# Performance work log

Measured on AMD Instinct MI355X. Metric: run time of the kernel, lower is better.

## Reference

```python
import jax, jax.numpy as jnp
import numpy as np
import math

D_SINGLE, D_PAIR, H, PQ, PV = 384, 128, 12, 4, 8
DH = D_SINGLE // H
OUT_DIM = H * DH + H * PV * 4 + H * D_PAIR


def setup_inputs() -> dict:
    key = jax.random.key(0)
    ks = jax.random.split(key, 24)
    B, L = 1, 512
    inp = {
        'single': jax.random.normal(ks[0], (B, L, D_SINGLE), jnp.float32),
        'pair': jax.random.normal(ks[1], (B, L, L, D_PAIR), jnp.float32),
        'rot_mats': jax.random.normal(ks[2], (B, L, 3, 3), jnp.float32),
        'trans': jax.random.normal(ks[3], (B, L, 3), jnp.float32),
        'mask': jnp.ones((B, L), jnp.float32),
        'ln_w': jnp.ones((D_SINGLE,), jnp.float32),
        'ln_b': jnp.zeros((D_SINGLE,), jnp.float32),
        'Wq': jax.random.normal(ks[4], (D_SINGLE, H * DH), jnp.float32) * 0.02,
        'bq': jnp.zeros((H * DH,), jnp.float32),
        'Wk': jax.random.normal(ks[5], (D_SINGLE, H * DH), jnp.float32) * 0.02,
        'bk': jnp.zeros((H * DH,), jnp.float32),
        'Wv': jax.random.normal(ks[6], (D_SINGLE, H * DH), jnp.float32) * 0.02,
        'bv': jnp.zeros((H * DH,), jnp.float32),
        'Wqp': jax.random.normal(ks[7], (D_SINGLE, H * PQ * 3), jnp.float32) * 0.02,
        'bqp': jnp.zeros((H * PQ * 3,), jnp.float32),
        'Wkp': jax.random.normal(ks[8], (D_SINGLE, H * PQ * 3), jnp.float32) * 0.02,
        'bkp': jnp.zeros((H * PQ * 3,), jnp.float32),
        'Wvp': jax.random.normal(ks[9], (D_SINGLE, H * PV * 3), jnp.float32) * 0.02,
        'bvp': jnp.zeros((H * PV * 3,), jnp.float32),
        'Wpb': jax.random.normal(ks[10], (D_PAIR, H), jnp.float32) * 0.02,
        'bpb': jnp.zeros((H,), jnp.float32),
        'Wo': jax.random.normal(ks[11], (OUT_DIM, D_SINGLE), jnp.float32) * 0.02,
        'bo': jnp.zeros((D_SINGLE,), jnp.float32),
        'w_c': jnp.asarray(1.0 / math.sqrt(3.0), jnp.float32),
        'w_l': jnp.asarray(1.0 / 3.0, jnp.float32),
        'gamma_h': jnp.ones((H,), jnp.float32),
    }
    return inp


def _layer_norm(x, w, b, eps=1e-5):
    mu = jnp.mean(x, axis=-1, keepdims=True)
    var = jnp.mean((x - mu) ** 2, axis=-1, keepdims=True)
    return (x - mu) * jax.lax.rsqrt(var + eps) * w + b


def reference(single, pair, rot_mats, trans, mask, ln_w, ln_b, Wq, bq, Wk, bk, Wv, bv,
              Wqp, bqp, Wkp, bkp, Wvp, bvp, Wpb, bpb, Wo, bo, w_c, w_l, gamma_h):
    B, L, _ = single.shape
    sn = _layer_norm(single, ln_w, ln_b)
    q = (sn @ Wq + bq).reshape(B, L, H, DH)
    k = (sn @ Wk + bk).reshape(B, L, H, DH)
    v = (sn @ Wv + bv).reshape(B, L, H, DH)
    qp = (sn @ Wqp + bqp).reshape(B, L, H, PQ, 3)
    kp = (sn @ Wkp + bkp).reshape(B, L, H, PQ, 3)
    vp = (sn @ Wvp + bvp).reshape(B, L, H, PV, 3)

    t = trans[:, :, None, None, :]  # [B,L,1,1,3]
    qg = jnp.einsum('blij,blhpj->blhpi', rot_mats, qp) + t
    kg = jnp.einsum('blij,blhpj->blhpi', rot_mats, kp) + t
    vg = jnp.einsum('blij,blhpj->blhpi', rot_mats, vp) + t

    # sequence logits [B,H,L,L]
    seq_logits = jnp.einsum('bihd,bjhd->bhij', q, k) * w_c / math.sqrt(DH)

    # geometric logits: pairwise point distances [B,H,L,L]
    q_pts = jnp.transpose(qg, (0, 2, 1, 3, 4))  # [B,H,L,PQ,3]
    k_pts = jnp.transpose(kg, (0, 2, 1, 3, 4))
    diff = q_pts[:, :, :, None] - k_pts[:, :, None]  # [B,H,L,L,PQ,3]
    dist_sq = jnp.sum(diff ** 2, axis=-1)            # [B,H,L,L,PQ]
    geo_logits = -0.5 * jnp.sum(dist_sq, axis=-1) * gamma_h[None, :, None, None] * w_l

    pair_bias = jnp.transpose(pair @ Wpb + bpb, (0, 3, 1, 2))  # [B,H,L,L]
    logits = seq_logits + geo_logits + pair_bias

    mask_2d = (mask[:, :, None] * mask[:, None, :])[:, None]  # [B,1,L,L]
    logits = jnp.where(mask_2d > 0, logits, jnp.float32(-1e9))
    attn = jax.nn.softmax(logits, axis=-1)  # [B,H,L,L]

    # sequence aggregation -> [B,L,H,DH]
    seq_out = jnp.einsum('bhij,bjhd->bihd', attn, v).reshape(B, L, H * DH)

    # point aggregation -> local frame features
    pts_out = jnp.einsum('bhij,bjhpd->bihpd', attn, vg)  # [B,L,H,PV,3]
    pts_local = jnp.einsum('blji,blhpj->blhpi', rot_mats, pts_out - t)
    pts_norm = jnp.linalg.norm(pts_local, axis=-1, keepdims=True)
    pts_feat = jnp.concatenate([pts_norm, pts_local], axis=-1).reshape(B, L, H * PV * 4)

    # pair aggregation -> [B,L,H*D_PAIR]
    pair_out = jnp.einsum('bhij,bijd->bihd', attn, pair).reshape(B, L, H * D_PAIR)

    combined = jnp.concatenate([seq_out, pts_feat, pair_out], axis=-1)
    return combined @ Wo + bo
```

## Files before the change

kernel.cpp:

```cpp
#include <hip/hip_runtime.h>
#include <math.h>

#define LQ    512
#define DS    384
#define DPAIR 128
#define NH    12
#define NPP   1792
#define FE    48
#define TJC   64
#define NC    8

__global__ void k_concat_w(const float* __restrict__ Wq, const float* __restrict__ Wk,
                           const float* __restrict__ Wv, const float* __restrict__ Wqp,
                           const float* __restrict__ Wkp, const float* __restrict__ Wvp,
                           const float* __restrict__ bq, const float* __restrict__ bk,
                           const float* __restrict__ bv, const float* __restrict__ bqp,
                           const float* __restrict__ bkp, const float* __restrict__ bvp,
                           float* __restrict__ Wcat, float* __restrict__ bcat) {
  int idx = blockIdx.x * 256 + threadIdx.x;
  const int total = DS * NPP;
  if (idx < total) {
    int k = idx / NPP, c = idx % NPP;
    float v = 0.f;
    if (c < 384)       v = Wq[k*384 + c];
    else if (c < 768)  v = Wk[k*384 + c-384];
    else if (c < 1152) v = Wv[k*384 + c-768];
    else if (c < 1296) v = Wqp[k*144 + c-1152];
    else if (c < 1440) v = Wkp[k*144 + c-1296];
    else if (c < 1728) v = Wvp[k*288 + c-1440];
    Wcat[idx] = v;
  } else if (idx < total + NPP) {
    int c = idx - total;
    float v = 0.f;
    if (c < 384)       v = bq[c];
    else if (c < 768)  v = bk[c-384];
    else if (c < 1152) v = bv[c-768];
    else if (c < 1296) v = bqp[c-1152];
    else if (c < 1440) v = bkp[c-1296];
    else if (c < 1728) v = bvp[c-1440];
    bcat[c] = v;
  }
}

__global__ void k_wpbt(const float* __restrict__ Wpb, float* __restrict__ WpbT) {
  int e = blockIdx.x * 256 + threadIdx.x;
  if (e >= DPAIR * NH) return;
  int k = e / NH, h = e % NH;
  WpbT[h*DPAIR + k] = Wpb[e];
}

__global__ __launch_bounds__(128) void k_layernorm(const float* __restrict__ x,
                                                   const float* __restrict__ w,
                                                   const float* __restrict__ b,
                                                   float* __restrict__ y) {
  __shared__ float red[128];
  __shared__ float s_mu, s_rstd;
  int i = blockIdx.x, t = threadIdx.x;
  float v0 = x[i*DS + t], v1 = x[i*DS + t + 128], v2 = x[i*DS + t + 256];
  red[t] = v0 + v1 + v2; __syncthreads();
  for (int s = 64; s > 0; s >>= 1) { if (t < s) red[t] += red[t+s]; __syncthreads(); }
  if (t == 0) s_mu = red[0] * (1.f/384.f);
  __syncthreads();
  float mu = s_mu;
  float d0 = v0-mu, d1 = v1-mu, d2 = v2-mu;
  red[t] = d0*d0 + d1*d1 + d2*d2; __syncthreads();
  for (int s = 64; s > 0; s >>= 1) { if (t < s) red[t] += red[t+s]; __syncthreads(); }
  if (t == 0) s_rstd = rsqrtf(red[0] * (1.f/384.f) + 1e-5f);
  __syncthreads();
  float r = s_rstd;
  y[i*DS + t      ] = d0*r*w[t      ] + b[t      ];
  y[i*DS + t + 128] = d1*r*w[t + 128] + b[t + 128];
  y[i*DS + t + 256] = d2*r*w[t + 256] + b[t + 256];
}

__global__ __launch_bounds__(256) void k_gemm_nn(const float* __restrict__ A,
                                                 const float* __restrict__ B,
                                                 const float* __restrict__ bias,
                                                 float* __restrict__ C,
                                                 float* __restrict__ Cpart,
                                                 int M, int N, int K) {
  __shared__ float As[16*68];
  __shared__ float Bs[16*68];
  int t = threadIdx.x;
  int mg = t >> 4, ng = t & 15;
  int i0 = blockIdx.y * 64, j0 = blockIdx.x * 64;
  int KS = gridDim.z;
  int kper = K / KS;
  int kbeg = blockIdx.z * kper;
  float acc[4][4] = {};
  for (int k0 = kbeg; k0 < kbeg + kper; k0 += 16) {
    int e = t;
    #pragma unroll
    for (int s = 0; s < 4; s++, e += 256) {
      int m = e >> 4, k = e & 15;
      As[k*68 + m] = A[(size_t)(i0+m)*K + k0 + k];
      int k2 = e >> 6, n = e & 63;
      Bs[k2*68 + n] = B[(size_t)(k0+k2)*N + j0 + n];
    }
    __syncthreads();
    #pragma unroll
    for (int k = 0; k < 16; k++) {
      float4 av = *(const float4*)(As + k*68 + mg*4);
      float4 bv = *(const float4*)(Bs + k*68 + ng*4);
      float a[4] = {av.x, av.y, av.z, av.w};
      float b[4] = {bv.x, bv.y, bv.z, bv.w};
      #pragma unroll
      for (int y = 0; y < 4; y++)
        #pragma unroll
        for (int x = 0; x < 4; x++)
          acc[y][x] = fmaf(a[y], b[x], acc[y][x]);
    }
    __syncthreads();
  }
  if (KS == 1) {
    #pragma unroll
    for (int y = 0; y < 4; y++) {
      int m = i0 + mg*4 + y;
      #pragma unroll
      for (int x = 0; x < 4; x++) {
        int n = j0 + ng*4 + x;
        C[(size_t)m*N + n] = acc[y][x] + bias[n];
      }
    }
  } else {
    float* dst = Cpart + (size_t)blockIdx.z * M * N;
    #pragma unroll
    for (int y = 0; y < 4; y++) {
      int m = i0 + mg*4 + y;
      #pragma unroll
      for (int x = 0; x < 4; x++) {
        int n = j0 + ng*4 + x;
        dst[(size_t)m*N + n] = acc[y][x];
      }
    }
  }
}

__global__ void k_reduce_bias(const float* __restrict__ part, const float* __restrict__ bias,
                              float* __restrict__ out, int MN, int N, int KS) {
  int e = blockIdx.x * 256 + threadIdx.x;
  if (e >= MN) return;
  float s = bias[e % N];
  for (int z = 0; z < KS; z++) s += part[(size_t)z*MN + e];
  out[e] = s;
}

__global__ void k_rotate(const float* __restrict__ C1, const float* __restrict__ rot,
                         const float* __restrict__ trans, float* __restrict__ qg,
                         float* __restrict__ kg, float* __restrict__ vg) {
  int idx = blockIdx.x * 256 + threadIdx.x;
  if (idx >= LQ*NH*16) return;
  int w = idx & 15; int h = (idx >> 4) % NH; int i = idx / (16*NH);
  const float* R = rot + (size_t)i*9;
  const float* tr = trans + (size_t)i*3;
  const float* src; float* dst;
  if (w < 4)      { src = C1 + (size_t)i*NPP + 1152 + h*12 + w*3;     dst = qg + ((size_t)i*NH + h)*12 + w*3; }
  else if (w < 8) { int p = w-4; src = C1 + (size_t)i*NPP + 1296 + h*12 + p*3; dst = kg + ((size_t)i*NH + h)*12 + p*3; }
  else            { int p = w-8; src = C1 + (size_t)i*NPP + 1440 + h*24 + p*3; dst = vg + ((size_t)i*NH + h)*24 + p*3; }
  float x = src[0], y = src[1], z = src[2];
  dst[0] = fmaf(R[0],x, fmaf(R[1],y, fmaf(R[2],z, tr[0])));
  dst[1] = fmaf(R[3],x, fmaf(R[4],y, fmaf(R[5],z, tr[1])));
  dst[2] = fmaf(R[6],x, fmaf(R[7],y, fmaf(R[8],z, tr[2])));
}

__global__ void k_features(const float* __restrict__ C1, const float* __restrict__ qg,
                           const float* __restrict__ kg, const float* __restrict__ gamma,
                           const float* __restrict__ w_c, const float* __restrict__ w_l,
                           float* __restrict__ Af, float* __restrict__ Bf) {
  int idx = blockIdx.x * 256 + threadIdx.x;
  if (idx >= LQ*NH) return;
  int h = idx % NH, i = idx / NH;
  float s  = w_c[0] * rsqrtf(32.f);
  float gp = gamma[h] * w_l[0];
  float* a  = Af + ((size_t)h*LQ + i)*FE;
  float* bb = Bf + ((size_t)h*LQ + i)*FE;
  const float* q = C1 + (size_t)i*NPP + h*32;
  const float* k = C1 + (size_t)i*NPP + 384 + h*32;
  for (int d = 0; d < 32; d++) { a[d] = s*q[d]; bb[d] = k[d]; }
  const float* qp = qg + ((size_t)i*NH + h)*12;
  const float* kp = kg + ((size_t)i*NH + h)*12;
  float sq = 0.f, sk = 0.f;
  for (int d = 0; d < 12; d++) {
    float x = qp[d], y = kp[d];
    a[32+d] = gp*x; bb[32+d] = y;
    sq = fmaf(x,x,sq); sk = fmaf(y,y,sk);
  }
  a[44] = -0.5f*gp*sq; a[45] = 1.f; a[46] = 0.f; a[47] = 0.f;
  bb[44] = 1.f; bb[45] = -0.5f*gp*sk; bb[46] = 0.f; bb[47] = 0.f;
}

__global__ __launch_bounds__(256) void k_logits_nt(const float* __restrict__ Af,
                                                   const float* __restrict__ Bf,
                                                   float* __restrict__ S) {
  __shared__ float As[48*68];
  __shared__ float Bs[48*68];
  int h = blockIdx.z;
  int i0 = blockIdx.y * 64, j0 = blockIdx.x * 64;
  int t = threadIdx.x;
  int mg = t >> 4, ng = t & 15;
  const float* Ah = Af + (size_t)h*LQ*FE;
  const float* Bh = Bf + (size_t)h*LQ*FE;
  for (int e = t; e < 64*48; e += 256) {
    int m = e / 48, k = e % 48;
    As[k*68 + m] = Ah[(size_t)(i0+m)*FE + k];
    Bs[k*68 + m] = Bh[(size_t)(j0+m)*FE + k];
  }
  __syncthreads();
  float acc[4][4] = {};
  #pragma unroll 8
  for (int k = 0; k < 48; k++) {
    float4 av = *(const float4*)(As + k*68 + mg*4);
    float4 bv = *(const float4*)(Bs + k*68 + ng*4);
    float a[4] = {av.x, av.y, av.z, av.w};
    float b[4] = {bv.x, bv.y, bv.z, bv.w};
    #pragma unroll
    for (int y = 0; y < 4; y++)
      #pragma unroll
      for (int x = 0; x < 4; x++)
        acc[y][x] = fmaf(a[y], b[x], acc[y][x]);
  }
  #pragma unroll
  for (int y = 0; y < 4; y++) {
    #pragma unroll
    for (int x = 0; x < 4; x++)
      S[((size_t)h*LQ + i0 + mg*4 + y)*LQ + j0 + ng*4 + x] = acc[y][x];
  }
}

__global__ __launch_bounds__(256, 4) void k_pair_chunk(
    const float* __restrict__ pair, const float* __restrict__ WpbT,
    const float* __restrict__ bpb, const float* __restrict__ mask,
    float* __restrict__ S, float* __restrict__ pairpart, float* __restrict__ msum) {
  __shared__ float tile[TJC*133];
  __shared__ float wt[NH*TJC];
  int i = blockIdx.x, c = blockIdx.y, t = threadIdx.x;
  int j0 = c*TJC;

  const float4* src = (const float4*)(pair + ((size_t)i*LQ + j0)*DPAIR);
  #pragma unroll
  for (int u = 0; u < 8; u++) {
    int e = t + u*256; int row = e >> 5, c4 = e & 31;
    *(float4*)&tile[row*133 + c4*4] = src[e];
  }

  int j = t & 63;
  int hg = __builtin_amdgcn_readfirstlane(t >> 6);
  int h0 = hg*3;
  float l[3];
  #pragma unroll
  for (int q = 0; q < 3; q++)
    l[q] = S[((size_t)(h0+q)*LQ + i)*LQ + j0 + j] + bpb[h0+q];
  bool dead = (mask[i] * mask[j0 + j] <= 0.f);
  __syncthreads();

  {
    const float* w0p = WpbT + (size_t)(h0+0)*DPAIR;
    const float* w1p = WpbT + (size_t)(h0+1)*DPAIR;
    const float* w2p = WpbT + (size_t)(h0+2)*DPAIR;
    float a0 = 0.f, a1 = 0.f, a2 = 0.f;
    #pragma unroll 8
    for (int k = 0; k < DPAIR; k += 4) {
      float4 pv = *(const float4*)&tile[j*133 + k];
      float4 w0 = *(const float4*)(w0p + k);
      float4 w1 = *(const float4*)(w1p + k);
      float4 w2 = *(const float4*)(w2p + k);
      a0 = fmaf(pv.x,w0.x, fmaf(pv.y,w0.y, fmaf(pv.z,w0.z, fmaf(pv.w,w0.w, a0))));
      a1 = fmaf(pv.x,w1.x, fmaf(pv.y,w1.y, fmaf(pv.z,w1.z, fmaf(pv.w,w1.w, a1))));
      a2 = fmaf(pv.x,w2.x, fmaf(pv.y,w2.y, fmaf(pv.z,w2.z, fmaf(pv.w,w2.w, a2))));
    }
    l[0] += a0; l[1] += a1; l[2] += a2;
    if (dead) { l[0] = -1e9f; l[1] = -1e9f; l[2] = -1e9f; }
  }

  #pragma unroll
  for (int q = 0; q < 3; q++) {
    float m = l[q];
    #pragma unroll
    for (int o = 32; o > 0; o >>= 1) m = fmaxf(m, __shfl_xor(m, o, 64));
    float w = __expf(l[q] - m);
    float sm = w;
    #pragma unroll
    for (int o = 32; o > 0; o >>= 1) sm += __shfl_xor(sm, o, 64);
    wt[(h0+q)*TJC + j] = w;
    S[((size_t)(h0+q)*LQ + i)*LQ + j0 + j] = w;
    if (j == 0) {
      float* dst = msum + (((size_t)i*NC + c)*NH + h0 + q)*2;
      dst[0] = m; dst[1] = sm;
    }
  }
  __syncthreads();

  int dg = t & 31, strip = t >> 5, jb = strip*8;
  float4 pv[8];
  #pragma unroll
  for (int q = 0; q < 8; q++) pv[q] = *(const float4*)&tile[(jb+q)*133 + dg*4];
  float4 acc[NH];
  #pragma unroll
  for (int h = 0; h < NH; h++) acc[h] = make_float4(0.f,0.f,0.f,0.f);
  #pragma unroll
  for (int h = 0; h < NH; h++) {
    float4 w0 = *(const float4*)&wt[h*TJC + jb];
    float4 w1 = *(const float4*)&wt[h*TJC + jb + 4];
    float wq[8] = {w0.x,w0.y,w0.z,w0.w,w1.x,w1.y,w1.z,w1.w};
    float4 a = acc[h];
    #pragma unroll
    for (int q = 0; q < 8; q++) {
      a.x = fmaf(wq[q], pv[q].x, a.x);
      a.y = fmaf(wq[q], pv[q].y, a.y);
      a.z = fmaf(wq[q], pv[q].z, a.z);
      a.w = fmaf(wq[q], pv[q].w, a.w);
    }
    acc[h] = a;
  }
  __syncthreads();

  float4* red4 = (float4*)tile;
  float4 tot[2];
  tot[0] = make_float4(0.f,0.f,0.f,0.f);
  tot[1] = make_float4(0.f,0.f,0.f,0.f);
  #pragma unroll
  for (int half = 0; half < 2; half++) {
    if ((strip >> 2) == half) {
      #pragma unroll
      for (int h = 0; h < NH; h++)
        red4[(((strip & 3)*NH) + h)*32 + dg] = acc[h];
    }
    __syncthreads();
    for (int e = t, u = 0; e < NH*32; e += 256, u++) {
      int rh = e >> 5, rd = e & 31;
      #pragma unroll
      for (int s4 = 0; s4 < 4; s4++) {
        float4 v = red4[((s4*NH) + rh)*32 + rd];
        tot[u].x += v.x; tot[u].y += v.y; tot[u].z += v.z; tot[u].w += v.w;
      }
    }
    __syncthreads();
  }
  for (int e = t, u = 0; e < NH*32; e += 256, u++) {
    int rh = e >> 5, rd = e & 31;
    *(float4*)&pairpart[(((size_t)i*NC + c)*NH + rh)*DPAIR + rd*4] = tot[u];
  }
}

__global__ __launch_bounds__(512) void k_merge(
    const float* __restrict__ msum, const float* __restrict__ pairpart,
    float* __restrict__ S, float* __restrict__ comb) {
  __shared__ float scs[NH*NC];
  int i = blockIdx.x, t = threadIdx.x;
  if (t < NH) {
    float m = -3.0e38f;
    float mc[NC], sc_[NC];
    #pragma unroll
    for (int c = 0; c < NC; c++) {
      const float* p = msum + (((size_t)i*NC + c)*NH + t)*2;
      mc[c] = p[0]; sc_[c] = p[1];
      m = fmaxf(m, mc[c]);
    }
    float s = 0.f;
    #pragma unroll
    for (int c = 0; c < NC; c++) s += sc_[c] * __expf(mc[c] - m);
    float inv = 1.f / s;
    #pragma unroll
    for (int c = 0; c < NC; c++) scs[t*NC + c] = __expf(mc[c] - m) * inv;
  }
  __syncthreads();
  if (t < NH*32) {
    int h = t >> 5, d = t & 31;
    float4 tot = make_float4(0.f,0.f,0.f,0.f);
    #pragma unroll
    for (int c = 0; c < NC; c++) {
      float sc = scs[h*NC + c];
      float4 v = *(const float4*)&pairpart[(((size_t)i*NC + c)*NH + h)*DPAIR + d*4];
      tot.x = fmaf(v.x, sc, tot.x); tot.y = fmaf(v.y, sc, tot.y);
      tot.z = fmaf(v.z, sc, tot.z); tot.w = fmaf(v.w, sc, tot.w);
    }
    *(float4*)&comb[(size_t)i*2304 + 768 + h*DPAIR + d*4] = tot;
  }
  for (int e = t; e < NH*LQ; e += 512) {
    int h = e >> 9, j = e & 511;
    size_t idx = ((size_t)h*LQ + i)*LQ + j;
    S[idx] *= scs[h*NC + (j >> 6)];
  }
}

__global__ __launch_bounds__(256) void k_attn_v(const float* __restrict__ attn,
                                                const float* __restrict__ C1,
                                                const float* __restrict__ vg,
                                                float* __restrict__ psum) {
  __shared__ float As[64*68];
  __shared__ float Vs[64*68];
  int i0 = blockIdx.x * 64;
  int h = blockIdx.y;
  int z = blockIdx.z;
  int t = threadIdx.x;
  int mg = t >> 4, ng = t & 15;
  float acc[4][4] = {};
  for (int k0 = z*128; k0 < z*128 + 128; k0 += 64) {
    __syncthreads();
    for (int e = t; e < 64*64; e += 256) {
      int m = e >> 6, j = e & 63;
      As[j*68 + m] = attn[((size_t)h*LQ + i0 + m)*LQ + k0 + j];
    }
    for (int e = t; e < 64*64; e += 256) {
      int j = e >> 6, c = e & 63;
      float v = 0.f;
      if (c < 32)      v = C1[(size_t)(k0+j)*NPP + 768 + h*32 + c];
      else if (c < 56) v = vg[((size_t)(k0+j)*NH + h)*24 + (c-32)];
      Vs[j*68 + c] = v;
    }
    __syncthreads();
    #pragma unroll 4
    for (int j = 0; j < 64; j++) {
      float4 av = *(const float4*)(As + j*68 + mg*4);
      float4 bv = *(const float4*)(Vs + j*68 + ng*4);
      float a[4] = {av.x, av.y, av.z, av.w};
      float b[4] = {bv.x, bv.y, bv.z, bv.w};
      #pragma unroll
      for (int y = 0; y < 4; y++)
        #pragma unroll
        for (int x = 0; x < 4; x++)
          acc[y][x] = fmaf(a[y], b[x], acc[y][x]);
    }
  }
  #pragma unroll
  for (int y = 0; y < 4; y++) {
    int i = i0 + mg*4 + y;
    #pragma unroll
    for (int x = 0; x < 4; x++) {
      int n = ng*4 + x;
      psum[(((size_t)z*LQ + i)*NH + h)*64 + n] = acc[y][x];
    }
  }
}

__global__ void k_av_reduce(const float* __restrict__ psum, float* __restrict__ comb,
                            float* __restrict__ pts) {
  int e = blockIdx.x * 256 + threadIdx.x;
  if (e >= LQ*NH*56) return;
  int n = e % 56; int ih = e / 56; int h = ih % NH; int i = ih / NH;
  size_t base = ((size_t)i*NH + h)*64 + n;
  float s = 0.f;
  for (int z = 0; z < 4; z++) s += psum[(size_t)z*LQ*NH*64 + base];
  if (n < 32) comb[(size_t)i*2304 + h*32 + n] = s;
  else        pts[((size_t)i*NH + h)*24 + (n-32)] = s;
}

__global__ void k_pts_feat(const float* __restrict__ pts, const float* __restrict__ rot,
                           const float* __restrict__ trans, float* __restrict__ comb) {
  int idx = blockIdx.x * 256 + threadIdx.x;
  if (idx >= LQ*NH*8) return;
  int p = idx & 7; int h = (idx >> 3) % NH; int i = idx / (8*NH);
  const float* R = rot + (size_t)i*9;
  const float* tr = trans + (size_t)i*3;
  const float* pt = pts + ((size_t)i*NH + h)*24 + p*3;
  float x = pt[0]-tr[0], y = pt[1]-tr[1], z = pt[2]-tr[2];
  float lx = fmaf(R[0],x, fmaf(R[3],y, R[6]*z));
  float ly = fmaf(R[1],x, fmaf(R[4],y, R[7]*z));
  float lz = fmaf(R[2],x, fmaf(R[5],y, R[8]*z));
  float nrm = sqrtf(fmaf(lx,lx, fmaf(ly,ly, lz*lz)));
  float* dst = comb + (size_t)i*2304 + 384 + (h*8 + p)*4;
  dst[0] = nrm; dst[1] = lx; dst[2] = ly; dst[3] = lz;
}

extern "C" void kernel_launch(void* const* d_in, const int* in_sizes, int n_in,
                              void* d_out, int out_size, void* d_ws, size_t ws_size,
                              hipStream_t stream) {
  const float* single = (const float*)d_in[0];
  const float* pair   = (const float*)d_in[1];
  const float* rot    = (const float*)d_in[2];
  const float* trans  = (const float*)d_in[3];
  const float* mask   = (const float*)d_in[4];
  const float* ln_w   = (const float*)d_in[5];
  const float* ln_b   = (const float*)d_in[6];
  const float* Wq     = (const float*)d_in[7];
  const float* bq     = (const float*)d_in[8];
  const float* Wk     = (const float*)d_in[9];
  const float* bk     = (const float*)d_in[10];
  const float* Wv     = (const float*)d_in[11];
  const float* bv     = (const float*)d_in[12];
  const float* Wqp    = (const float*)d_in[13];
  const float* bqp    = (const float*)d_in[14];
  const float* Wkp    = (const float*)d_in[15];
  const float* bkp    = (const float*)d_in[16];
  const float* Wvp    = (const float*)d_in[17];
  const float* bvp    = (const float*)d_in[18];
  const float* Wpb    = (const float*)d_in[19];
  const float* bpb    = (const float*)d_in[20];
  const float* Wo     = (const float*)d_in[21];
  const float* bo     = (const float*)d_in[22];
  const float* w_c    = (const float*)d_in[23];
  const float* w_l    = (const float*)d_in[24];
  const float* gamma  = (const float*)d_in[25];
  float* out = (float*)d_out;

  float* p = (float*)d_ws;
  auto alloc = [&](size_t n) { float* r = p; p += n; return r; };
  float* Wcat    = alloc((size_t)DS*NPP);
  float* bcat    = alloc(NPP);
  float* WpbT    = alloc((size_t)NH*DPAIR);
  float* sn      = alloc((size_t)LQ*DS);
  float* C1      = alloc((size_t)LQ*NPP);
  float* qg      = alloc((size_t)LQ*NH*12);
  float* kg      = alloc((size_t)LQ*NH*12);
  float* vgb     = alloc((size_t)LQ*NH*24);
  float* Af      = alloc((size_t)NH*LQ*FE);
  float* Bf      = alloc((size_t)NH*LQ*FE);
  float* S       = alloc((size_t)NH*LQ*LQ);
  float* pairpart= alloc((size_t)LQ*NC*NH*DPAIR);
  float* msum    = alloc((size_t)LQ*NC*NH*2);
  float* comb    = alloc((size_t)LQ*2304);
  float* pts     = alloc((size_t)LQ*NH*24);
  float* scratch = alloc((size_t)8*LQ*DS);

  k_concat_w<<<dim3((DS*NPP + NPP + 255)/256), 256, 0, stream>>>(
      Wq, Wk, Wv, Wqp, Wkp, Wvp, bq, bk, bv, bqp, bkp, bvp, Wcat, bcat);
  k_wpbt<<<dim3((DPAIR*NH + 255)/256), 256, 0, stream>>>(Wpb, WpbT);
  k_layernorm<<<dim3(LQ), 128, 0, stream>>>(single, ln_w, ln_b, sn);
  k_gemm_nn<<<dim3(NPP/64, LQ/64, 1), 256, 0, stream>>>(sn, Wcat, bcat, C1, nullptr, LQ, NPP, DS);
  k_rotate<<<dim3((LQ*NH*16 + 255)/256), 256, 0, stream>>>(C1, rot, trans, qg, kg, vgb);
  k_features<<<dim3((LQ*NH + 255)/256), 256, 0, stream>>>(C1, qg, kg, gamma, w_c, w_l, Af, Bf);
  k_logits_nt<<<dim3(LQ/64, LQ/64, NH), 256, 0, stream>>>(Af, Bf, S);
  k_pair_chunk<<<dim3(LQ, NC), 256, 0, stream>>>(pair, WpbT, bpb, mask, S, pairpart, msum);
  k_merge<<<dim3(LQ), 512, 0, stream>>>(msum, pairpart, S, comb);
  k_attn_v<<<dim3(LQ/64, NH, 4), 256, 0, stream>>>(S, C1, vgb, scratch);
  k_av_reduce<<<dim3((LQ*NH*56 + 255)/256), 256, 0, stream>>>(scratch, comb, pts);
  k_pts_feat<<<dim3((LQ*NH*8 + 255)/256), 256, 0, stream>>>(pts, rot, trans, comb);
  k_gemm_nn<<<dim3(DS/64, LQ/64, 8), 256, 0, stream>>>(comb, Wo, bo, nullptr, scratch, LQ, DS, 2304);
  k_reduce_bias<<<dim3((LQ*DS + 255)/256), 256, 0, stream>>>(scratch, bo, out, LQ*DS, DS, 8);
}
```

Measured before the change: 386.6 us.

## Fuse small kernels and fold softmax chunk rescale into attention-V load

Merges the Wpb transpose into the weight-concat kernel, fuses rotation with feature building, and fuses the AV reduction with the point-feature transform, so fewer launches and intermediate buffers are needed. The merge kernel no longer rewrites the full L×L×H attention matrix to apply per-chunk softmax scales. Instead the scales are stored compactly and applied as attention tiles are loaded in the AV GEMM, which removes one full read and write of S. It also splits the first projection GEMM over K=2 with a separate bias reduction and lowers k_pair_chunk's occupancy hint from 4 to 2, which adds a reduction pass and may change register use.

```diff
diff --git a/kernel.cpp b/kernel.cpp
--- a/kernel.cpp
+++ b/kernel.cpp
@@ -16,7 +16,9 @@
                            const float* __restrict__ bq, const float* __restrict__ bk,
                            const float* __restrict__ bv, const float* __restrict__ bqp,
                            const float* __restrict__ bkp, const float* __restrict__ bvp,
-                           float* __restrict__ Wcat, float* __restrict__ bcat) {
+                           const float* __restrict__ Wpb,
+                           float* __restrict__ Wcat, float* __restrict__ bcat,
+                           float* __restrict__ WpbT) {
   int idx = blockIdx.x * 256 + threadIdx.x;
   const int total = DS * NPP;
   if (idx < total) {
@@ -39,14 +41,11 @@
     else if (c < 1440) v = bkp[c-1296];
     else if (c < 1728) v = bvp[c-1440];
     bcat[c] = v;
-  }
-}
-
-__global__ void k_wpbt(const float* __restrict__ Wpb, float* __restrict__ WpbT) {
-  int e = blockIdx.x * 256 + threadIdx.x;
-  if (e >= DPAIR * NH) return;
-  int k = e / NH, h = e % NH;
-  WpbT[h*DPAIR + k] = Wpb[e];
+  } else if (idx < total + NPP + DPAIR*NH) {
+    int e = idx - total - NPP;
+    int k = e / NH, h = e % NH;
+    WpbT[h*DPAIR + k] = Wpb[e];
+  }
 }
 
 __global__ __launch_bounds__(128) void k_layernorm(const float* __restrict__ x,
@@ -145,48 +144,61 @@
   out[e] = s;
 }
 
-__global__ void k_rotate(const float* __restrict__ C1, const float* __restrict__ rot,
-                         const float* __restrict__ trans, float* __restrict__ qg,
-                         float* __restrict__ kg, float* __restrict__ vg) {
-  int idx = blockIdx.x * 256 + threadIdx.x;
-  if (idx >= LQ*NH*16) return;
-  int w = idx & 15; int h = (idx >> 4) % NH; int i = idx / (16*NH);
-  const float* R = rot + (size_t)i*9;
-  const float* tr = trans + (size_t)i*3;
-  const float* src; float* dst;
-  if (w < 4)      { src = C1 + (size_t)i*NPP + 1152 + h*12 + w*3;     dst = qg + ((size_t)i*NH + h)*12 + w*3; }
-  else if (w < 8) { int p = w-4; src = C1 + (size_t)i*NPP + 1296 + h*12 + p*3; dst = kg + ((size_t)i*NH + h)*12 + p*3; }
-  else            { int p = w-8; src = C1 + (size_t)i*NPP + 1440 + h*24 + p*3; dst = vg + ((size_t)i*NH + h)*24 + p*3; }
-  float x = src[0], y = src[1], z = src[2];
-  dst[0] = fmaf(R[0],x, fmaf(R[1],y, fmaf(R[2],z, tr[0])));
-  dst[1] = fmaf(R[3],x, fmaf(R[4],y, fmaf(R[5],z, tr[1])));
-  dst[2] = fmaf(R[6],x, fmaf(R[7],y, fmaf(R[8],z, tr[2])));
-}
-
-__global__ void k_features(const float* __restrict__ C1, const float* __restrict__ qg,
-                           const float* __restrict__ kg, const float* __restrict__ gamma,
-                           const float* __restrict__ w_c, const float* __restrict__ w_l,
-                           float* __restrict__ Af, float* __restrict__ Bf) {
+__global__ void k_rotfeat(const float* __restrict__ C1, const float* __restrict__ rot,
+                          const float* __restrict__ trans, const float* __restrict__ gamma,
+                          const float* __restrict__ w_c, const float* __restrict__ w_l,
+                          float* __restrict__ Af, float* __restrict__ Bf,
+                          float* __restrict__ vgb) {
   int idx = blockIdx.x * 256 + threadIdx.x;
   if (idx >= LQ*NH) return;
   int h = idx % NH, i = idx / NH;
+  float R[9], tr[3];
+  #pragma unroll
+  for (int r = 0; r < 9; r++) R[r] = rot[(size_t)i*9 + r];
+  #pragma unroll
+  for (int r = 0; r < 3; r++) tr[r] = trans[(size_t)i*3 + r];
+
   float s  = w_c[0] * rsqrtf(32.f);
   float gp = gamma[h] * w_l[0];
   float* a  = Af + ((size_t)h*LQ + i)*FE;
   float* bb = Bf + ((size_t)h*LQ + i)*FE;
   const float* q = C1 + (size_t)i*NPP + h*32;
   const float* k = C1 + (size_t)i*NPP + 384 + h*32;
+  #pragma unroll 8
   for (int d = 0; d < 32; d++) { a[d] = s*q[d]; bb[d] = k[d]; }
-  const float* qp = qg + ((size_t)i*NH + h)*12;
-  const float* kp = kg + ((size_t)i*NH + h)*12;
+
+  const float* qp = C1 + (size_t)i*NPP + 1152 + h*12;
+  const float* kp = C1 + (size_t)i*NPP + 1296 + h*12;
   float sq = 0.f, sk = 0.f;
-  for (int d = 0; d < 12; d++) {
-    float x = qp[d], y = kp[d];
-    a[32+d] = gp*x; bb[32+d] = y;
-    sq = fmaf(x,x,sq); sk = fmaf(y,y,sk);
+  #pragma unroll
+  for (int p = 0; p < 4; p++) {
+    float x = qp[p*3], y = qp[p*3+1], z = qp[p*3+2];
+    #pragma unroll
+    for (int r = 0; r < 3; r++) {
+      float g = fmaf(R[r*3],x, fmaf(R[r*3+1],y, fmaf(R[r*3+2],z, tr[r])));
+      a[32 + p*3 + r] = gp*g;
+      sq = fmaf(g,g,sq);
+    }
+    float xk = kp[p*3], yk = kp[p*3+1], zk = kp[p*3+2];
+    #pragma unroll
+    for (int r = 0; r < 3; r++) {
+      float g = fmaf(R[r*3],xk, fmaf(R[r*3+1],yk, fmaf(R[r*3+2],zk, tr[r])));
+      bb[32 + p*3 + r] = g;
+      sk = fmaf(g,g,sk);
+    }
   }
   a[44] = -0.5f*gp*sq; a[45] = 1.f; a[46] = 0.f; a[47] = 0.f;
   bb[44] = 1.f; bb[45] = -0.5f*gp*sk; bb[46] = 0.f; bb[47] = 0.f;
+
+  const float* vp = C1 + (size_t)i*NPP + 1440 + h*24;
+  float* vd = vgb + ((size_t)i*NH + h)*24;
+  #pragma unroll
+  for (int p = 0; p < 8; p++) {
+    float x = vp[p*3], y = vp[p*3+1], z = vp[p*3+2];
+    #pragma unroll
+    for (int r = 0; r < 3; r++)
+      vd[p*3 + r] = fmaf(R[r*3],x, fmaf(R[r*3+1],y, fmaf(R[r*3+2],z, tr[r])));
+  }
 }
 
 __global__ __launch_bounds__(256) void k_logits_nt(const float* __restrict__ Af,
@@ -227,7 +239,7 @@
   }
 }
 
-__global__ __launch_bounds__(256, 4) void k_pair_chunk(
+__global__ __launch_bounds__(256, 2) void k_pair_chunk(
     const float* __restrict__ pair, const float* __restrict__ WpbT,
     const float* __restrict__ bpb, const float* __restrict__ mask,
     float* __restrict__ S, float* __restrict__ pairpart, float* __restrict__ msum) {
@@ -342,9 +354,9 @@
   }
 }
 
-__global__ __launch_bounds__(512) void k_merge(
+__global__ __launch_bounds__(384) void k_scs_pairout(
     const float* __restrict__ msum, const float* __restrict__ pairpart,
-    float* __restrict__ S, float* __restrict__ comb) {
+    float* __restrict__ scs_g, float* __restrict__ comb) {
   __shared__ float scs[NH*NC];
   int i = blockIdx.x, t = threadIdx.x;
   if (t < NH) {
@@ -361,31 +373,29 @@
     for (int c = 0; c < NC; c++) s += sc_[c] * __expf(mc[c] - m);
     float inv = 1.f / s;
     #pragma unroll
-    for (int c = 0; c < NC; c++) scs[t*NC + c] = __expf(mc[c] - m) * inv;
-  }
-  __syncthreads();
-  if (t < NH*32) {
-    int h = t >> 5, d = t & 31;
-    float4 tot = make_float4(0.f,0.f,0.f,0.f);
-    #pragma unroll
     for (int c = 0; c < NC; c++) {
-      float sc = scs[h*NC + c];
-      float4 v = *(const float4*)&pairpart[(((size_t)i*NC + c)*NH + h)*DPAIR + d*4];
-      tot.x = fmaf(v.x, sc, tot.x); tot.y = fmaf(v.y, sc, tot.y);
-      tot.z = fmaf(v.z, sc, tot.z); tot.w = fmaf(v.w, sc, tot.w);
-    }
-    *(float4*)&comb[(size_t)i*2304 + 768 + h*DPAIR + d*4] = tot;
-  }
-  for (int e = t; e < NH*LQ; e += 512) {
-    int h = e >> 9, j = e & 511;
-    size_t idx = ((size_t)h*LQ + i)*LQ + j;
-    S[idx] *= scs[h*NC + (j >> 6)];
-  }
+      float v = __expf(mc[c] - m) * inv;
+      scs[t*NC + c] = v;
+      scs_g[((size_t)i*NH + t)*NC + c] = v;
+    }
+  }
+  __syncthreads();
+  int h = t >> 5, d = t & 31;
+  float4 tot = make_float4(0.f,0.f,0.f,0.f);
+  #pragma unroll
+  for (int c = 0; c < NC; c++) {
+    float sc = scs[h*NC + c];
+    float4 v = *(const float4*)&pairpart[(((size_t)i*NC + c)*NH + h)*DPAIR + d*4];
+    tot.x = fmaf(v.x, sc, tot.x); tot.y = fmaf(v.y, sc, tot.y);
+    tot.z = fmaf(v.z, sc, tot.z); tot.w = fmaf(v.w, sc, tot.w);
+  }
+  *(float4*)&comb[(size_t)i*2304 + 768 + h*DPAIR + d*4] = tot;
 }
 
 __global__ __launch_bounds__(256) void k_attn_v(const float* __restrict__ attn,
                                                 const float* __restrict__ C1,
                                                 const float* __restrict__ vg,
+                                                const float* __restrict__ scs,
                                                 float* __restrict__ psum) {
   __shared__ float As[64*68];
   __shared__ float Vs[64*68];
@@ -396,17 +406,19 @@
   int mg = t >> 4, ng = t & 15;
   float acc[4][4] = {};
   for (int k0 = z*128; k0 < z*128 + 128; k0 += 64) {
+    int c = k0 >> 6;
     __syncthreads();
     for (int e = t; e < 64*64; e += 256) {
       int m = e >> 6, j = e & 63;
-      As[j*68 + m] = attn[((size_t)h*LQ + i0 + m)*LQ + k0 + j];
+      float sc = scs[((size_t)(i0+m)*NH + h)*NC + c];
+      As[j*68 + m] = attn[((size_t)h*LQ + i0 + m)*LQ + k0 + j] * sc;
     }
     for (int e = t; e < 64*64; e += 256) {
-      int j = e >> 6, c = e & 63;
+      int j = e >> 6, cc = e & 63;
       float v = 0.f;
-      if (c < 32)      v = C1[(size_t)(k0+j)*NPP + 768 + h*32 + c];
-      else if (c < 56) v = vg[((size_t)(k0+j)*NH + h)*24 + (c-32)];
-      Vs[j*68 + c] = v;
+      if (cc < 32)      v = C1[(size_t)(k0+j)*NPP + 768 + h*32 + cc];
+      else if (cc < 56) v = vg[((size_t)(k0+j)*NH + h)*24 + (cc-32)];
+      Vs[j*68 + cc] = v;
     }
     __syncthreads();
     #pragma unroll 4
@@ -433,33 +445,36 @@
   }
 }
 
-__global__ void k_av_reduce(const float* __restrict__ psum, float* __restrict__ comb,
-                            float* __restrict__ pts) {
-  int e = blockIdx.x * 256 + threadIdx.x;
-  if (e >= LQ*NH*56) return;
-  int n = e % 56; int ih = e / 56; int h = ih % NH; int i = ih / NH;
-  size_t base = ((size_t)i*NH + h)*64 + n;
-  float s = 0.f;
-  for (int z = 0; z < 4; z++) s += psum[(size_t)z*LQ*NH*64 + base];
-  if (n < 32) comb[(size_t)i*2304 + h*32 + n] = s;
-  else        pts[((size_t)i*NH + h)*24 + (n-32)] = s;
-}
-
-__global__ void k_pts_feat(const float* __restrict__ pts, const float* __restrict__ rot,
-                           const float* __restrict__ trans, float* __restrict__ comb) {
+__global__ void k_avpts(const float* __restrict__ psum, const float* __restrict__ rot,
+                        const float* __restrict__ trans, float* __restrict__ comb) {
   int idx = blockIdx.x * 256 + threadIdx.x;
-  if (idx >= LQ*NH*8) return;
-  int p = idx & 7; int h = (idx >> 3) % NH; int i = idx / (8*NH);
-  const float* R = rot + (size_t)i*9;
-  const float* tr = trans + (size_t)i*3;
-  const float* pt = pts + ((size_t)i*NH + h)*24 + p*3;
-  float x = pt[0]-tr[0], y = pt[1]-tr[1], z = pt[2]-tr[2];
-  float lx = fmaf(R[0],x, fmaf(R[3],y, R[6]*z));
-  float ly = fmaf(R[1],x, fmaf(R[4],y, R[7]*z));
-  float lz = fmaf(R[2],x, fmaf(R[5],y, R[8]*z));
-  float nrm = sqrtf(fmaf(lx,lx, fmaf(ly,ly, lz*lz)));
-  float* dst = comb + (size_t)i*2304 + 384 + (h*8 + p)*4;
-  dst[0] = nrm; dst[1] = lx; dst[2] = ly; dst[3] = lz;
+  if (idx >= LQ*NH*40) return;
+  int w = idx % 40; int ih = idx / 40; int h = ih % NH; int i = ih / NH;
+  size_t base = ((size_t)i*NH + h)*64;
+  if (w < 32) {
+    float s = 0.f;
+    for (int z = 0; z < 4; z++) s += psum[(size_t)z*LQ*NH*64 + base + w];
+    comb[(size_t)i*2304 + h*32 + w] = s;
+  } else {
+    int p = w - 32;
+    float g[3];
+    #pragma unroll
+    for (int r = 0; r < 3; r++) {
+      int n = 32 + p*3 + r;
+      float s = 0.f;
+      for (int z = 0; z < 4; z++) s += psum[(size_t)z*LQ*NH*64 + base + n];
+      g[r] = s;
+    }
+    const float* R = rot + (size_t)i*9;
+    const float* tr = trans + (size_t)i*3;
+    float x = g[0]-tr[0], y = g[1]-tr[1], z = g[2]-tr[2];
+    float lx = fmaf(R[0],x, fmaf(R[3],y, R[6]*z));
+    float ly = fmaf(R[1],x, fmaf(R[4],y, R[7]*z));
+    float lz = fmaf(R[2],x, fmaf(R[5],y, R[8]*z));
+    float nrm = sqrtf(fmaf(lx,lx, fmaf(ly,ly, lz*lz)));
+    float* dst = comb + (size_t)i*2304 + 384 + (h*8 + p)*4;
+    dst[0] = nrm; dst[1] = lx; dst[2] = ly; dst[3] = lz;
+  }
 }
 
 extern "C" void kernel_launch(void* const* d_in, const int* in_sizes, int n_in,
@@ -500,31 +515,27 @@
   float* WpbT    = alloc((size_t)NH*DPAIR);
   float* sn      = alloc((size_t)LQ*DS);
   float* C1      = alloc((size_t)LQ*NPP);
-  float* qg      = alloc((size_t)LQ*NH*12);
-  float* kg      = alloc((size_t)LQ*NH*12);
   float* vgb     = alloc((size_t)LQ*NH*24);
   float* Af      = alloc((size_t)NH*LQ*FE);
   float* Bf      = alloc((size_t)NH*LQ*FE);
   float* S       = alloc((size_t)NH*LQ*LQ);
   float* pairpart= alloc((size_t)LQ*NC*NH*DPAIR);
   float* msum    = alloc((size_t)LQ*NC*NH*2);
+  float* scs_g   = alloc((size_t)LQ*NH*NC);
   float* comb    = alloc((size_t)LQ*2304);
-  float* pts     = alloc((size_t)LQ*NH*24);
-  float* scratch = alloc((size_t)8*LQ*DS);
-
-  k_concat_w<<<dim3((DS*NPP + NPP + 255)/256), 256, 0, stream>>>(
-      Wq, Wk, Wv, Wqp, Wkp, Wvp, bq, bk, bv, bqp, bkp, bvp, Wcat, bcat);
-  k_wpbt<<<dim3((DPAIR*NH + 255)/256), 256, 0, stream>>>(Wpb, WpbT);
+  float* scratch = alloc((size_t)2*LQ*NPP);
+
+  k_concat_w<<<dim3((DS*NPP + NPP + DPAIR*NH + 255)/256), 256, 0, stream>>>(
+      Wq, Wk, Wv, Wqp, Wkp, Wvp, bq, bk, bv, bqp, bkp, bvp, Wpb, Wcat, bcat, WpbT);
   k_layernorm<<<dim3(LQ), 128, 0, stream>>>(single, ln_w, ln_b, sn);
-  k_gemm_nn<<<dim3(NPP/64, LQ/64, 1), 256, 0, stream>>>(sn, Wcat, bcat, C1, nullptr, LQ, NPP, DS);
-  k_rotate<<<dim3((LQ*NH*16 + 255)/256), 256, 0, stream>>>(C1, rot, trans, qg, kg, vgb);
-  k_features<<<dim3((LQ*NH + 255)/256), 256, 0, stream>>>(C1, qg, kg, gamma, w_c, w_l, Af, Bf);
+  k_gemm_nn<<<dim3(NPP/64, LQ/64, 2), 256, 0, stream>>>(sn, Wcat, nullptr, nullptr, scratch, LQ, NPP, DS);
+  k_reduce_bias<<<dim3((LQ*NPP + 255)/256), 256, 0, stream>>>(scratch, bcat, C1, LQ*NPP, NPP, 2);
+  k_rotfeat<<<dim3((LQ*NH + 255)/256), 256, 0, stream>>>(C1, rot, trans, gamma, w_c, w_l, Af, Bf, vgb);
   k_logits_nt<<<dim3(LQ/64, LQ/64, NH), 256, 0, stream>>>(Af, Bf, S);
   k_pair_chunk<<<dim3(LQ, NC), 256, 0, stream>>>(pair, WpbT, bpb, mask, S, pairpart, msum);
-  k_merge<<<dim3(LQ), 512, 0, stream>>>(msum, pairpart, S, comb);
-  k_attn_v<<<dim3(LQ/64, NH, 4), 256, 0, stream>>>(S, C1, vgb, scratch);
-  k_av_reduce<<<dim3((LQ*NH*56 + 255)/256), 256, 0, stream>>>(scratch, comb, pts);
-  k_pts_feat<<<dim3((LQ*NH*8 + 255)/256), 256, 0, stream>>>(pts, rot, trans, comb);
-  k_gemm_nn<<<dim3(DS/64, LQ/64, 8), 256, 0, stream>>>(comb, Wo, bo, nullptr, scratch, LQ, DS, 2304);
+  k_scs_pairout<<<dim3(LQ), 384, 0, stream>>>(msum, pairpart, scs_g, comb);
+  k_attn_v<<<dim3(LQ/64, NH, 4), 256, 0, stream>>>(S, C1, vgb, scs_g, scratch);
+  k_avpts<<<dim3((LQ*NH*40 + 255)/256), 256, 0, stream>>>(scratch, rot, trans, comb);
+  k_gemm_nn<<<dim3(DS/64, LQ/64, 8), 256, 0, stream>>>(comb, Wo, nullptr, nullptr, scratch, LQ, DS, 2304);
   k_reduce_bias<<<dim3((LQ*DS + 255)/256), 256, 0, stream>>>(scratch, bo, out, LQ*DS, DS, 8);
 }
```

Result: no change. 379.3 us (-1.9%).
